# Performance work log

Hardware: AMD Instinct MI355X
Metric: run time of the kernel (lower is better)

Reference implementation:

```python
import jax, jax.numpy as jnp
import numpy as np

D = 256  # rst_input_dim


def _gru_cell(x, h, W_ih, W_hh, b_ih, b_hh):
    # x, h: (..., D); W_*: (3D, D); PyTorch GRU gate order: r, z, n
    gi = x @ W_ih.T + b_ih          # (..., 3D)
    gh = h @ W_hh.T + b_hh
    i_r, i_z, i_n = jnp.split(gi, 3, axis=-1)
    h_r, h_z, h_n = jnp.split(gh, 3, axis=-1)
    r = jax.nn.sigmoid(i_r + h_r)
    z = jax.nn.sigmoid(i_z + h_z)
    n = jnp.tanh(i_n + r * h_n)
    return (1.0 - z) * n + z * h


def setup_inputs() -> dict:
    key = jax.random.key(0)
    ks = jax.random.split(key, 5)
    B, L = 32, 4096
    s = 1.0 / np.sqrt(D)
    return {
        "leaf_embeds": jax.random.normal(ks[0], (B, L, D), dtype=jnp.float32),
        "W_ih": jax.random.normal(ks[1], (3 * D, D), dtype=jnp.float32) * s,
        "W_hh": jax.random.normal(ks[2], (3 * D, D), dtype=jnp.float32) * s,
        "b_ih": jax.random.normal(ks[3], (3 * D,), dtype=jnp.float32) * s,
        "b_hh": jax.random.normal(ks[4], (3 * D,), dtype=jnp.float32) * s,
    }


def reference(leaf_embeds, W_ih, W_hh, b_ih, b_hh):
    # Post-order traversal of a perfect binary tree, batched level-by-level
    # (classic tree-RNN same-depth batching). Leaves: embed = EDU embedding,
    # hidden = zeros. Internal node: h0 = mean(h_left, h_right); run GRU over
    # the 2-step sequence [left_embed, right_embed]; out = mean of the two
    # GRU outputs; returned hidden = final GRU hidden.
    embeds = leaf_embeds                      # (B, N, D)
    hs = jnp.zeros_like(leaf_embeds)          # (B, N, D)
    n = embeds.shape[1]
    while n > 1:
        xL, xR = embeds[:, 0::2], embeds[:, 1::2]   # (B, n/2, D)
        hL, hR = hs[:, 0::2], hs[:, 1::2]
        h0 = 0.5 * (hL + hR)                         # mean of child hiddens
        h1 = _gru_cell(xL, h0, W_ih, W_hh, b_ih, b_hh)
        h2 = _gru_cell(xR, h1, W_ih, W_hh, b_ih, b_hh)
        embeds = 0.5 * (h1 + h2)                     # mean over seq outputs
        hs = h2
        n //= 2
    return embeds[:, 0]                              # (B, D): root embedding
```

## Files before the change

kernel.cpp:

```cpp
#include <hip/hip_runtime.h>
#include <hip/hip_bf16.h>
#include <stdint.h>

typedef _Float16 f16x8 __attribute__((ext_vector_type(8)));
typedef float    f32x4 __attribute__((ext_vector_type(4)));

#define GLDS16(gptr, lptr) \
  __builtin_amdgcn_global_load_lds((const __attribute__((address_space(1))) void*)(gptr), \
                                   (__attribute__((address_space(3))) void*)(lptr), 16, 0, 0)

#define WAITV(N) asm volatile("s_waitcnt vmcnt(" #N ")" ::: "memory")

__device__ __forceinline__ int tile_off(int rb, int c, int sub) {
    return ((rb * 4 + c) * 8 + sub) * 512;
}

__global__ __launch_bounds__(256) void prepack_weights(
    const float* __restrict__ Wih, const float* __restrict__ Whh,
    const float* __restrict__ bih, const float* __restrict__ bhh,
    _Float16* __restrict__ WP, float* __restrict__ BC)
{
    if (blockIdx.x == 2048) {
        int i = threadIdx.x;
        BC[i]       = bih[i] + bhh[i];
        BC[256 + i] = bih[256 + i] + bhh[256 + i];
        BC[512 + i] = bih[512 + i];
        BC[768 + i] = bhh[512 + i];
        return;
    }
    int idx = blockIdx.x * 256 + threadIdx.x;
    int j   = idx & 7;
    int nl  = (idx >> 3) & 63;
    int sub = (idx >> 9) & 7;
    int g   = (idx >> 12) & 3;
    int d0b = (idx >> 14) & 3;
    int c   = idx >> 16;
    int k = c * 64 + sub * 8 + j;
    int d = d0b * 64 + nl;
    float v = 0.f;
    if (g == 0)      v = (k < 256) ? Wih[d * 256 + k]         : Whh[d * 256 + (k - 256)];
    else if (g == 1) v = (k < 256) ? Wih[(256 + d) * 256 + k] : Whh[(256 + d) * 256 + (k - 256)];
    else if (g == 2) v = (k < 256) ? Wih[(512 + d) * 256 + k] : 0.f;
    else             v = (k >= 256) ? Whh[(512 + d) * 256 + (k - 256)] : 0.f;
    WP[idx] = (_Float16)v;
}

__global__ __launch_bounds__(256) void convert_split(
    const float* __restrict__ leaf, _Float16* __restrict__ XE, _Float16* __restrict__ XO)
{
    int g = blockIdx.x * 256 + threadIdx.x;
    int u = g & 31;
    int row = g >> 5;
    const float* src = leaf + (size_t)row * 256 + u * 8;
    float4 a = *(const float4*)src;
    float4 b = *(const float4*)(src + 4);
    f16x8 p;
    p[0] = (_Float16)a.x; p[1] = (_Float16)a.y; p[2] = (_Float16)a.z; p[3] = (_Float16)a.w;
    p[4] = (_Float16)b.x; p[5] = (_Float16)b.y; p[6] = (_Float16)b.z; p[7] = (_Float16)b.w;
    int ro = row >> 1;
    _Float16* dst = (row & 1) ? XO : XE;
    *(f16x8*)(dst + tile_off(ro >> 6, u >> 3, u & 7) + (ro & 63) * 8) = p;
}

template<int MT, bool SWIZ>
__global__ __launch_bounds__(256, (MT == 8) ? 2 : 3) void gru_cell(
    const _Float16* __restrict__ Xsrc,
    const _Float16* __restrict__ Hsrc,
    const _Float16* __restrict__ WP,
    const float* __restrict__ BC,
    _Float16* __restrict__ Hout,
    _Float16* __restrict__ Ee, _Float16* __restrict__ Eo, _Float16* __restrict__ HP,
    int M)
{
    (void)M;
    constexpr int NBUF = (MT == 8) ? 2 : 3;
    constexpr int AROW = MT * 16 * 8;
    constexpr int ASZ  = 8 * AROW;
    constexpr int BROW = 512;
    constexpr int BSZ  = 3 * 8 * BROW;
    __shared__ __align__(16) _Float16 Alds[NBUF * ASZ];
    __shared__ __align__(16) _Float16 Blds[NBUF * BSZ];

    const int tid  = threadIdx.x;
    int bm, d0b;
    if (SWIZ) {
        int xcd = blockIdx.x & 7, slot = blockIdx.x >> 3;
        d0b = slot & 3;
        bm  = (slot >> 2) * 8 + xcd;
    } else {
        bm = blockIdx.x >> 2; d0b = blockIdx.x & 3;
    }
    const int wave = tid >> 6, lane = tid & 63;
    const int quad = lane >> 4, lo = lane & 15;

    const bool has_h = (Hsrc != nullptr);
    const int nch = has_h ? 8 : 4;

    f32x4 acc[MT][4];
#pragma unroll
    for (int a = 0; a < MT; ++a)
#pragma unroll
        for (int b = 0; b < 4; ++b) acc[a][b] = (f32x4){0.f, 0.f, 0.f, 0.f};
    float hinv[MT][4];

    auto issueB = [&](int c, int buf) {
        const size_t cb = (size_t)(c * 4 + d0b) * 4;
        _Float16* dstb = Blds + buf * BSZ;
#pragma unroll
        for (int i = 0; i < 6; ++i) {
            int bi = wave * 6 + i;
            int slot = bi >> 3, sub = bi & 7;
            int g = (slot == 2) ? ((c < 4) ? 2 : 3) : slot;
            GLDS16(WP + ((cb + g) * 8 + sub) * 512 + lane * 8,
                   dstb + (slot * 8 + sub) * BROW);
        }
    };

    auto issueA = [&](int c, int buf) {
        const _Float16* base = (c < 4) ? Xsrc : Hsrc;
        const int cc = c & 3;
        _Float16* Ab = Alds + buf * ASZ;
        constexpr int ND = MT / 2;
#pragma unroll
        for (int i = 0; i < ND; ++i) {
            int ai = wave * ND + i;
            int sub = (MT == 8) ? (ai >> 1) : ai;
            int mh  = (MT == 8) ? (ai & 1) : 0;
            GLDS16(base + tile_off(bm * (MT / 4) + mh, cc, sub) + lane * 8,
                   Ab + sub * AROW + mh * 512);
        }
    };

    auto compute = [&](int c, int buf) {
        const _Float16* Bb = Blds + buf * BSZ;
        const _Float16* Ab = Alds + buf * ASZ;
#pragma unroll
        for (int ks = 0; ks < 2; ++ks) {
            const int subb = ks * 4 + quad;
            const _Float16* brow = Bb + subb * BROW + (wave * 16 + lo) * 8;
            f16x8 b0 = *(const f16x8*)(brow);
            f16x8 b1 = *(const f16x8*)(brow + 8 * BROW);
            f16x8 b2 = *(const f16x8*)(brow + 16 * BROW);
            f16x8 af[MT];
#pragma unroll
            for (int mt = 0; mt < MT; ++mt)
                af[mt] = *(const f16x8*)(Ab + subb * AROW + (mt * 16 + lo) * 8);
#pragma unroll
            for (int mt = 0; mt < MT; ++mt)
                acc[mt][0] = __builtin_amdgcn_mfma_f32_16x16x32_f16(af[mt], b0, acc[mt][0], 0, 0, 0);
#pragma unroll
            for (int mt = 0; mt < MT; ++mt)
                acc[mt][1] = __builtin_amdgcn_mfma_f32_16x16x32_f16(af[mt], b1, acc[mt][1], 0, 0, 0);
            if (c < 4) {
#pragma unroll
                for (int mt = 0; mt < MT; ++mt)
                    acc[mt][2] = __builtin_amdgcn_mfma_f32_16x16x32_f16(af[mt], b2, acc[mt][2], 0, 0, 0);
            } else {
#pragma unroll
                for (int mt = 0; mt < MT; ++mt)
                    acc[mt][3] = __builtin_amdgcn_mfma_f32_16x16x32_f16(af[mt], b2, acc[mt][3], 0, 0, 0);
            }
        }
        if (has_h && c == 4 + d0b) {
            const _Float16* Ab2 = Alds + buf * ASZ;
            const int colw = wave * 16 + lo;
            const int sub = colw >> 3, j = colw & 7;
#pragma unroll
            for (int mt = 0; mt < MT; ++mt)
#pragma unroll
                for (int r = 0; r < 4; ++r)
                    hinv[mt][r] = (float)Ab2[sub * AROW + (mt * 16 + quad * 4 + r) * 8 + j];
        }
    };

    if constexpr (MT == 8) {
        issueB(0, 0);
        issueA(0, 0);
        for (int c = 0; c < nch; ++c) {
            __syncthreads();
            if (c + 1 < nch) {
                issueB(c + 1, (c + 1) & 1);
                issueA(c + 1, (c + 1) & 1);
            }
            compute(c, c & 1);
        }
    } else {
        issueB(0, 0); issueA(0, 0);
        issueB(1, 1); issueA(1, 1);
        for (int c = 0; c < nch; ++c) {
            if (c < nch - 1) WAITV(8); else WAITV(0);
            __builtin_amdgcn_s_barrier();
            __builtin_amdgcn_sched_barrier(0);
            if (c + 2 < nch) {
                int buf = (c + 2) % 3;
                issueB(c + 2, buf);
                issueA(c + 2, buf);
            }
            compute(c, c % 3);
        }
    }

    const int ld = wave * 16 + lo;
    const int d  = d0b * 64 + ld;
    const float brz0 = BC[d];
    const float brz1 = BC[256 + d];
    const float bni  = BC[512 + d];
    const float bnh  = BC[768 + d];
    constexpr int SROW = 72;
    constexpr int PR   = MT * 8;
    __syncthreads();
#pragma unroll
    for (int mt = 0; mt < MT; ++mt) {
        const int lr0 = mt * 16 + quad * 4;
        float hq[4];
#pragma unroll
        for (int r = 0; r < 4; ++r) {
            float hin = has_h ? hinv[mt][r] : 0.f;
            float rg = 1.f / (1.f + __expf(-(acc[mt][0][r] + brz0)));
            float zg = 1.f / (1.f + __expf(-(acc[mt][1][r] + brz1)));
            float ex = __expf(2.f * (acc[mt][2][r] + bni + rg * (acc[mt][3][r] + bnh)));
            float nv = 1.f - 2.f / (ex + 1.f);
            hq[r] = (1.f - zg) * nv + zg * hin;
            int lr = lr0 + r;
            if (Hout) {
                Alds[lr * SROW + ld] = (_Float16)hq[r];
            } else {
                Alds[(((lr & 1) * PR) + (lr >> 1)) * SROW + ld] =
                    (_Float16)(0.5f * (hin + hq[r]));
            }
        }
        if (!Hout) {
            Alds[(2 * PR + (lr0 >> 1)) * SROW + ld]     = (_Float16)(0.5f * (hq[0] + hq[1]));
            Alds[(2 * PR + (lr0 >> 1) + 1) * SROW + ld] = (_Float16)(0.5f * (hq[2] + hq[3]));
        }
    }
    __syncthreads();

    if (Hout) {
        constexpr int NU = MT * 128;
#pragma unroll
        for (int i = 0; i < NU / 256; ++i) {
            int uid = i * 256 + tid;
            int r = uid & 63, sub = (uid >> 6) & 7, mh = uid >> 9;
            f16x8 v = *(const f16x8*)&Alds[(mh * 64 + r) * SROW + sub * 8];
            *(f16x8*)(Hout + tile_off(bm * (MT / 4) + mh, d0b, sub) + r * 8) = v;
        }
    } else {
        constexpr int NU = 3 * PR * 8;
        const int rbE  = (MT == 8) ? bm : (bm >> 1);
        const int roff = (MT == 8) ? 0 : (bm & 1) * 32;
#pragma unroll
        for (int i = 0; i < NU / 256; ++i) {
            int uid = i * 256 + tid;
            int pr   = uid & (PR - 1);
            int rest = uid / PR;
            int sub = rest & 7, buf = rest >> 3;
            f16x8 v = *(const f16x8*)&Alds[(buf * PR + pr) * SROW + sub * 8];
            _Float16* dst = (buf == 0) ? Ee : (buf == 1) ? Eo : HP;
            *(f16x8*)(dst + tile_off(rbE, d0b, sub) + (roff + pr) * 8) = v;
        }
    }
}

__global__ __launch_bounds__(256) void final_out(
    const _Float16* __restrict__ XE, const _Float16* __restrict__ XO,
    float* __restrict__ out)
{
    int i = blockIdx.x * 256 + threadIdx.x;
    int j = i >> 8, col = i & 255;
    const _Float16* src = (j & 1) ? XO : XE;
    int r = j >> 1;
    out[i] = (float)src[tile_off(0, col >> 6, (col >> 3) & 7) + r * 8 + (col & 7)];
}

extern "C" void kernel_launch(void* const* d_in, const int* in_sizes, int n_in,
                              void* d_out, int out_size, void* d_ws, size_t ws_size,
                              hipStream_t stream) {
    const float* leaf = (const float*)d_in[0];
    const float* Wih  = (const float*)d_in[1];
    const float* Whh  = (const float*)d_in[2];
    const float* bih  = (const float*)d_in[3];
    const float* bhh  = (const float*)d_in[4];

    char* ws = (char*)d_ws;
    _Float16* WPp = (_Float16*)ws;
    _Float16* XAe = (_Float16*)(ws + (1ull  << 20));
    _Float16* XAo = (_Float16*)(ws + (33ull << 20));
    _Float16* XBe = (_Float16*)(ws + (65ull << 20));
    _Float16* XBo = (_Float16*)(ws + (81ull << 20));
    _Float16* H1  = (_Float16*)(ws + (97ull << 20));
    _Float16* HPb = (_Float16*)(ws + (129ull << 20));
    float*    BCp = (float*)(ws + (145ull << 20));

    prepack_weights<<<2049, 256, 0, stream>>>(Wih, Whh, bih, bhh, WPp, BCp);
    convert_split<<<16384, 256, 0, stream>>>(leaf, XAe, XAo);

    _Float16 *XeC = XAe, *XoC = XAo, *XeN = XBe, *XoN = XBo;
    const _Float16* hp = nullptr;
    int M = 65536;
    for (int lev = 0; lev < 12; ++lev) {
        if (M >= 8192) {
            int grid = (M / 128) * 4;
            gru_cell<8, true><<<grid, 256, 0, stream>>>(XeC, hp, WPp, BCp,
                                                        H1, nullptr, nullptr, nullptr, M);
            gru_cell<8, true><<<grid, 256, 0, stream>>>(XoC, H1, WPp, BCp,
                                                        nullptr, XeN, XoN, HPb, M);
        } else {
            int nbm = (M + 63) / 64;
            int grid = nbm * 4;
            if ((nbm & 7) == 0) {
                gru_cell<4, true><<<grid, 256, 0, stream>>>(XeC, hp, WPp, BCp,
                                                            H1, nullptr, nullptr, nullptr, M);
                gru_cell<4, true><<<grid, 256, 0, stream>>>(XoC, H1, WPp, BCp,
                                                            nullptr, XeN, XoN, HPb, M);
            } else {
                gru_cell<4, false><<<grid, 256, 0, stream>>>(XeC, hp, WPp, BCp,
                                                             H1, nullptr, nullptr, nullptr, M);
                gru_cell<4, false><<<grid, 256, 0, stream>>>(XoC, H1, WPp, BCp,
                                                             nullptr, XeN, XoN, HPb, M);
            }
        }
        hp = HPb;
        _Float16* t;
        t = XeC; XeC = XeN; XeN = t;
        t = XoC; XoC = XoN; XoN = t;
        M >>= 1;
    }
    final_out<<<32, 256, 0, stream>>>(XeC, XoC, (float*)d_out);
}
```

Measured before the change: 666.1 us.

## Load GRU weight fragments directly into registers instead of staging through LDS

Removes the shared-memory buffers for the weight tiles. Each wave now reads its B fragments straight from global memory into registers at the start of every chunk, and only the activation tiles go through async global-to-LDS copies; the vmcnt waits shrink to match. Hidden-state inputs are kept as half precision to save registers. This lowers LDS footprint and LDS traffic, which may allow more occupancy, but the weight loads are no longer prefetched a chunk ahead, so their global latency sits on the critical path before each chunk's MFMAs.

After: 662.9 us. Within noise of the previous version (-0.5%).

```diff
diff --git a/kernel.cpp b/kernel.cpp
--- a/kernel.cpp
+++ b/kernel.cpp
@@ -3,6 +3,7 @@
 #include <stdint.h>
 
 typedef _Float16 f16x8 __attribute__((ext_vector_type(8)));
+typedef _Float16 f16x4 __attribute__((ext_vector_type(4)));
 typedef float    f32x4 __attribute__((ext_vector_type(4)));
 
 #define GLDS16(gptr, lptr) \
@@ -76,10 +77,7 @@
     constexpr int NBUF = (MT == 8) ? 2 : 3;
     constexpr int AROW = MT * 16 * 8;
     constexpr int ASZ  = 8 * AROW;
-    constexpr int BROW = 512;
-    constexpr int BSZ  = 3 * 8 * BROW;
     __shared__ __align__(16) _Float16 Alds[NBUF * ASZ];
-    __shared__ __align__(16) _Float16 Blds[NBUF * BSZ];
 
     const int tid  = threadIdx.x;
     int bm, d0b;
@@ -101,18 +99,19 @@
     for (int a = 0; a < MT; ++a)
 #pragma unroll
         for (int b = 0; b < 4; ++b) acc[a][b] = (f32x4){0.f, 0.f, 0.f, 0.f};
-    float hinv[MT][4];
-
-    auto issueB = [&](int c, int buf) {
+    f16x4 hinvh[MT];
+
+    auto loadB = [&](int c, f16x8 (&bb)[2][3]) {
         const size_t cb = (size_t)(c * 4 + d0b) * 4;
-        _Float16* dstb = Blds + buf * BSZ;
-#pragma unroll
-        for (int i = 0; i < 6; ++i) {
-            int bi = wave * 6 + i;
-            int slot = bi >> 3, sub = bi & 7;
-            int g = (slot == 2) ? ((c < 4) ? 2 : 3) : slot;
-            GLDS16(WP + ((cb + g) * 8 + sub) * 512 + lane * 8,
-                   dstb + (slot * 8 + sub) * BROW);
+        const int col = (wave * 16 + lo) * 8;
+#pragma unroll
+        for (int ks = 0; ks < 2; ++ks) {
+            const int subb = ks * 4 + quad;
+#pragma unroll
+            for (int slot = 0; slot < 3; ++slot) {
+                int g = (slot == 2) ? ((c < 4) ? 2 : 3) : slot;
+                bb[ks][slot] = *(const f16x8*)(WP + ((cb + g) * 8 + subb) * 512 + col);
+            }
         }
     };
 
@@ -131,72 +130,54 @@
         }
     };
 
-    auto compute = [&](int c, int buf) {
-        const _Float16* Bb = Blds + buf * BSZ;
+    auto compute = [&](int c, int buf, f16x8 (&bb)[2][3]) {
         const _Float16* Ab = Alds + buf * ASZ;
 #pragma unroll
         for (int ks = 0; ks < 2; ++ks) {
             const int subb = ks * 4 + quad;
-            const _Float16* brow = Bb + subb * BROW + (wave * 16 + lo) * 8;
-            f16x8 b0 = *(const f16x8*)(brow);
-            f16x8 b1 = *(const f16x8*)(brow + 8 * BROW);
-            f16x8 b2 = *(const f16x8*)(brow + 16 * BROW);
-            f16x8 af[MT];
-#pragma unroll
-            for (int mt = 0; mt < MT; ++mt)
-                af[mt] = *(const f16x8*)(Ab + subb * AROW + (mt * 16 + lo) * 8);
-#pragma unroll
-            for (int mt = 0; mt < MT; ++mt)
-                acc[mt][0] = __builtin_amdgcn_mfma_f32_16x16x32_f16(af[mt], b0, acc[mt][0], 0, 0, 0);
-#pragma unroll
-            for (int mt = 0; mt < MT; ++mt)
-                acc[mt][1] = __builtin_amdgcn_mfma_f32_16x16x32_f16(af[mt], b1, acc[mt][1], 0, 0, 0);
-            if (c < 4) {
-#pragma unroll
-                for (int mt = 0; mt < MT; ++mt)
-                    acc[mt][2] = __builtin_amdgcn_mfma_f32_16x16x32_f16(af[mt], b2, acc[mt][2], 0, 0, 0);
-            } else {
-#pragma unroll
-                for (int mt = 0; mt < MT; ++mt)
-                    acc[mt][3] = __builtin_amdgcn_mfma_f32_16x16x32_f16(af[mt], b2, acc[mt][3], 0, 0, 0);
+#pragma unroll
+            for (int mt = 0; mt < MT; ++mt) {
+                f16x8 a = *(const f16x8*)(Ab + subb * AROW + (mt * 16 + lo) * 8);
+                acc[mt][0] = __builtin_amdgcn_mfma_f32_16x16x32_f16(a, bb[ks][0], acc[mt][0], 0, 0, 0);
+                acc[mt][1] = __builtin_amdgcn_mfma_f32_16x16x32_f16(a, bb[ks][1], acc[mt][1], 0, 0, 0);
+                if (c < 4)
+                    acc[mt][2] = __builtin_amdgcn_mfma_f32_16x16x32_f16(a, bb[ks][2], acc[mt][2], 0, 0, 0);
+                else
+                    acc[mt][3] = __builtin_amdgcn_mfma_f32_16x16x32_f16(a, bb[ks][2], acc[mt][3], 0, 0, 0);
             }
         }
         if (has_h && c == 4 + d0b) {
-            const _Float16* Ab2 = Alds + buf * ASZ;
             const int colw = wave * 16 + lo;
             const int sub = colw >> 3, j = colw & 7;
 #pragma unroll
             for (int mt = 0; mt < MT; ++mt)
 #pragma unroll
                 for (int r = 0; r < 4; ++r)
-                    hinv[mt][r] = (float)Ab2[sub * AROW + (mt * 16 + quad * 4 + r) * 8 + j];
+                    hinvh[mt][r] = Ab[sub * AROW + (mt * 16 + quad * 4 + r) * 8 + j];
         }
     };
 
     if constexpr (MT == 8) {
-        issueB(0, 0);
         issueA(0, 0);
         for (int c = 0; c < nch; ++c) {
             __syncthreads();
-            if (c + 1 < nch) {
-                issueB(c + 1, (c + 1) & 1);
-                issueA(c + 1, (c + 1) & 1);
-            }
-            compute(c, c & 1);
+            f16x8 bb[2][3];
+            loadB(c, bb);
+            __builtin_amdgcn_sched_barrier(0);
+            if (c + 1 < nch) issueA(c + 1, (c + 1) & 1);
+            compute(c, c & 1, bb);
         }
     } else {
-        issueB(0, 0); issueA(0, 0);
-        issueB(1, 1); issueA(1, 1);
+        issueA(0, 0); issueA(1, 1);
         for (int c = 0; c < nch; ++c) {
-            if (c < nch - 1) WAITV(8); else WAITV(0);
+            if (c < nch - 1) WAITV(2); else WAITV(0);
             __builtin_amdgcn_s_barrier();
             __builtin_amdgcn_sched_barrier(0);
-            if (c + 2 < nch) {
-                int buf = (c + 2) % 3;
-                issueB(c + 2, buf);
-                issueA(c + 2, buf);
-            }
-            compute(c, c % 3);
+            f16x8 bb[2][3];
+            loadB(c, bb);
+            __builtin_amdgcn_sched_barrier(0);
+            if (c + 2 < nch) issueA(c + 2, (c + 2) % 3);
+            compute(c, c % 3, bb);
         }
     }
 
@@ -215,7 +196,7 @@
         float hq[4];
 #pragma unroll
         for (int r = 0; r < 4; ++r) {
-            float hin = has_h ? hinv[mt][r] : 0.f;
+            float hin = has_h ? (float)hinvh[mt][r] : 0.f;
             float rg = 1.f / (1.f + __expf(-(acc[mt][0][r] + brz0)));
             float zg = 1.f / (1.f + __expf(-(acc[mt][1][r] + brz1)));
             float ex = __expf(2.f * (acc[mt][2][r] + bni + rg * (acc[mt][3][r] + bnh)));
```
